# Performance work log

Hardware: AMD Instinct MI355X
Metric: run time of the kernel (lower is better)

The kernel has to match this reference:

```python
import jax, jax.numpy as jnp
import numpy as np

NEG_SLOPE = 0.2

def gat_conv(x, src, dst, W, a_src, a_dst, b, heads, out_ch, num_nodes):
    # Linear projection per head: [N, H, C]
    h = (x @ W).reshape(num_nodes, heads, out_ch)
    # Per-node attention logits: [N, H]
    s_src = jnp.sum(h * a_src[None, :, :], axis=-1)
    s_dst = jnp.sum(h * a_dst[None, :, :], axis=-1)
    # Per-edge attention score, LeakyReLU(0.2): [E, H]
    e = jax.nn.leaky_relu(s_src[src] + s_dst[dst], negative_slope=NEG_SLOPE)
    # Segment softmax over incoming edges of each destination node
    e_max = jax.ops.segment_max(e, dst, num_segments=num_nodes)
    e_exp = jnp.exp(e - e_max[dst])
    denom = jax.ops.segment_sum(e_exp, dst, num_segments=num_nodes)
    alpha = e_exp / (denom[dst] + 1e-16)  # [E, H]
    # Weighted message aggregation: [N, H, C]
    msg = h[src] * alpha[:, :, None]
    out = jax.ops.segment_sum(msg, dst, num_segments=num_nodes)
    # Concat heads + bias
    return out.reshape(num_nodes, heads * out_ch) + b


def setup_inputs() -> dict:
    key = jax.random.key(0)
    ks = jax.random.split(key, 9)
    N, E = 50000, 1000000
    x = jax.random.normal(ks[0], (N, 300), dtype=jnp.float32)
    edge_index = jax.random.randint(ks[1], (2, E), 0, N, dtype=jnp.int64)
    W1 = jax.random.normal(ks[2], (300, 64), dtype=jnp.float32) * 0.05
    a_src1 = jax.random.normal(ks[3], (8, 8), dtype=jnp.float32) * 0.1
    a_dst1 = jax.random.normal(ks[4], (8, 8), dtype=jnp.float32) * 0.1
    b1 = jnp.zeros((64,), dtype=jnp.float32)
    W2 = jax.random.normal(ks[5], (64, 64), dtype=jnp.float32) * 0.1
    a_src2 = jax.random.normal(ks[6], (1, 64), dtype=jnp.float32) * 0.1
    a_dst2 = jax.random.normal(ks[7], (1, 64), dtype=jnp.float32) * 0.1
    b2 = jnp.zeros((64,), dtype=jnp.float32)
    return {"x": x, "edge_index": edge_index, "W1": W1, "a_src1": a_src1,
            "a_dst1": a_dst1, "b1": b1, "W2": W2, "a_src2": a_src2,
            "a_dst2": a_dst2, "b2": b2}


def reference(x, edge_index, W1, a_src1, a_dst1, b1, W2, a_src2, a_dst2, b2):
    N = x.shape[0]
    src, dst = edge_index[0], edge_index[1]
    # eval mode: dropouts are identity
    h = gat_conv(x, src, dst, W1, a_src1, a_dst1, b1, heads=8, out_ch=8, num_nodes=N)
    h = jax.nn.elu(h)
    out = gat_conv(h, src, dst, W2, a_src2, a_dst2, b2, heads=1, out_ch=64, num_nodes=N)
    return out
```

## Files before the change

kernel.cpp:

```cpp
#include <hip/hip_runtime.h>
#include <math.h>

#define NN 50000
#define NE 1000000
#define EC 31
#define ECP 32
#define CSH 15
#define WR 8
#define RNG 6250
#define RPAD 6272
#define NCNT (EC * WR)
#define NGB 782

typedef __bf16 bf16x8 __attribute__((ext_vector_type(8)));
typedef float f32x4 __attribute__((ext_vector_type(4)));

__device__ inline unsigned short f2bf(float f) {
    unsigned u = __float_as_uint(f);
    u += 0x7FFFu + ((u >> 16) & 1u);
    return (unsigned short)(u >> 16);
}
__device__ inline float bf2f(unsigned short s) {
    return __uint_as_float(((unsigned)s) << 16);
}
__device__ inline float bflo(unsigned r) { return __uint_as_float(r << 16); }
__device__ inline float bfhi(unsigned r) { return __uint_as_float(r & 0xffff0000u); }

__global__ __launch_bounds__(256) void prep_init(const float* __restrict__ W1,
        const float* __restrict__ W2, unsigned short* __restrict__ Bt1,
        unsigned short* __restrict__ Bt2)
{
    int t = blockIdx.x * 256 + threadIdx.x;
    if (t < 64 * 320) {
        int c = t / 320, k = t % 320;
        Bt1[t] = (k < 300) ? f2bf(W1[k * 64 + c]) : (unsigned short)0;
    } else {
        int i = t - 64 * 320;
        int c = i >> 6, k = i & 63;
        Bt2[i] = f2bf(W2[k * 64 + c]);
    }
}

__global__ __launch_bounds__(1024) void k_count(
        const int* __restrict__ ei, int* __restrict__ cnt,
        unsigned char* __restrict__ pos)
{
    __shared__ __align__(16) int sm[RNG];
    const int tid = threadIdx.x;
    const int bid = blockIdx.x;
    const int c = bid >> 3, w = bid & 7;
    const int lo = w * RNG;
    for (int j = tid; j < RNG; j += 1024) sm[j] = 0;
    __syncthreads();
    const int base = c << CSH;
    #pragma unroll
    for (int it = 0; it < (1 << CSH) / 4096; ++it) {
        int e = base + (it * 1024 + tid) * 4;
        if (e < NE) {
            int4 d = *(const int4*)(ei + NE + e);
            unsigned t0 = (unsigned)(d.x - lo), t1 = (unsigned)(d.y - lo);
            unsigned t2 = (unsigned)(d.z - lo), t3 = (unsigned)(d.w - lo);
            if (t0 < RNG) pos[e]     = (unsigned char)atomicAdd(&sm[t0], 1);
            if (t1 < RNG) pos[e + 1] = (unsigned char)atomicAdd(&sm[t1], 1);
            if (t2 < RNG) pos[e + 2] = (unsigned char)atomicAdd(&sm[t2], 1);
            if (t3 < RNG) pos[e + 3] = (unsigned char)atomicAdd(&sm[t3], 1);
        }
    }
    __syncthreads();
    int* dstp = cnt + (size_t)bid * RPAD;
    for (int j = tid; j < RNG; j += 1024) dstp[j] = sm[j];
}

__global__ __launch_bounds__(256) void k_gemm(
        const float* __restrict__ A, const unsigned short* __restrict__ Bt,
        unsigned short* __restrict__ hb,
        const float* __restrict__ asrc, const float* __restrict__ adst,
        float* __restrict__ ss, float* __restrict__ sd)
{
    __shared__ unsigned short lds[5120];
    const int tid = threadIdx.x;
    const int row0 = blockIdx.x * 64;
    const int lane = tid & 63, w = tid >> 6;
    const int quad = lane >> 4, mm = lane & 15;
    const int sr = tid >> 2, q8 = (tid & 3) * 8;
    const int gsr = row0 + sr;
    const int K = 300, KT = 10, Kpad = 320, M = NN;

    f32x4 acc[4];
    #pragma unroll
    for (int i = 0; i < 4; ++i) acc[i] = (f32x4){0.f, 0.f, 0.f, 0.f};

    for (int kt = 0; kt < KT; ++kt) {
        const int k0 = kt * 32;
        int4 apack = {0, 0, 0, 0};
        if (gsr < M) {
            const float* ap = A + (size_t)gsr * K + k0 + q8;
            unsigned short* up = (unsigned short*)&apack;
            if (k0 + q8 + 7 < K) {
                float4 v0 = *(const float4*)ap;
                float4 v1 = *(const float4*)(ap + 4);
                up[0]=f2bf(v0.x); up[1]=f2bf(v0.y); up[2]=f2bf(v0.z); up[3]=f2bf(v0.w);
                up[4]=f2bf(v1.x); up[5]=f2bf(v1.y); up[6]=f2bf(v1.z); up[7]=f2bf(v1.w);
            } else {
                #pragma unroll
                for (int j = 0; j < 8; ++j)
                    up[j] = (k0 + q8 + j < K) ? f2bf(ap[j]) : (unsigned short)0;
            }
        }
        *(int4*)(lds + sr * 40 + q8) = apack;
        *(int4*)(lds + 2560 + sr * 40 + q8) =
            *(const int4*)(Bt + (size_t)sr * Kpad + k0 + q8);
        __syncthreads();
        bf16x8 af = *(const bf16x8*)(lds + (w * 16 + mm) * 40 + quad * 8);
        #pragma unroll
        for (int nt = 0; nt < 4; ++nt) {
            bf16x8 bfv = *(const bf16x8*)(lds + 2560 + (nt * 16 + mm) * 40 + quad * 8);
            acc[nt] = __builtin_amdgcn_mfma_f32_16x16x32_bf16(af, bfv, acc[nt], 0, 0, 0);
        }
        __syncthreads();
    }
    #pragma unroll
    for (int nt = 0; nt < 4; ++nt)
        #pragma unroll
        for (int reg = 0; reg < 4; ++reg)
            lds[w * 1152 + (quad * 4 + reg) * 72 + nt * 16 + mm] = f2bf(acc[nt][reg]);
    __syncthreads();
    const int cg = (tid & 3) * 16;
    const unsigned short* crow = lds + (sr >> 4) * 1152 + (sr & 15) * 72;
    if (gsr < M) {
        *(int4*)(hb + (size_t)gsr * 64 + cg)     = *(const int4*)(crow + cg);
        *(int4*)(hb + (size_t)gsr * 64 + cg + 8) = *(const int4*)(crow + cg + 8);
    }
    #pragma unroll
    for (int hh = 0; hh < 2; ++hh) {
        int hd = (tid & 3) + hh * 4;
        float pss = 0.f, psd = 0.f;
        #pragma unroll
        for (int c = 0; c < 8; ++c) {
            float hv = bf2f(crow[hd * 8 + c]);
            pss += hv * asrc[hd * 8 + c];
            psd += hv * adst[hd * 8 + c];
        }
        if (gsr < M) { ss[gsr * 8 + hd] = pss; sd[gsr * 8 + hd] = psd; }
    }
}

__global__ __launch_bounds__(256) void gemm_l2(const unsigned short* __restrict__ A,
        const unsigned short* __restrict__ Bt, unsigned short* __restrict__ hb,
        const float* __restrict__ asrc, const float* __restrict__ adst,
        float* __restrict__ ss, float* __restrict__ sd)
{
    __shared__ unsigned short lds[5120];
    const int tid  = threadIdx.x;
    const int row0 = blockIdx.x * 64;
    const int lane = tid & 63, w = tid >> 6;
    const int quad = lane >> 4, mm = lane & 15;
    const int sr = tid >> 2, q8 = (tid & 3) * 8;
    const int gsr = row0 + sr;
    const int K = 64, KT = 2, Kpad = 64, M = NN;

    f32x4 acc[4];
    #pragma unroll
    for (int i = 0; i < 4; ++i) acc[i] = (f32x4){0.f, 0.f, 0.f, 0.f};

    for (int kt = 0; kt < KT; ++kt) {
        const int k0 = kt * 32;
        int4 apack = {0, 0, 0, 0};
        if (gsr < M) apack = *(const int4*)(A + (size_t)gsr * K + k0 + q8);
        *(int4*)(lds + sr * 40 + q8) = apack;
        *(int4*)(lds + 2560 + sr * 40 + q8) =
            *(const int4*)(Bt + (size_t)sr * Kpad + k0 + q8);
        __syncthreads();
        bf16x8 af = *(const bf16x8*)(lds + (w * 16 + mm) * 40 + quad * 8);
        #pragma unroll
        for (int nt = 0; nt < 4; ++nt) {
            bf16x8 bfv = *(const bf16x8*)(lds + 2560 + (nt * 16 + mm) * 40 + quad * 8);
            acc[nt] = __builtin_amdgcn_mfma_f32_16x16x32_bf16(af, bfv, acc[nt], 0, 0, 0);
        }
        __syncthreads();
    }
    #pragma unroll
    for (int nt = 0; nt < 4; ++nt)
        #pragma unroll
        for (int reg = 0; reg < 4; ++reg)
            lds[w * 1152 + (quad * 4 + reg) * 72 + nt * 16 + mm] = f2bf(acc[nt][reg]);
    __syncthreads();
    const int cg = (tid & 3) * 16;
    const unsigned short* crow = lds + (sr >> 4) * 1152 + (sr & 15) * 72;
    if (gsr < M) {
        *(int4*)(hb + (size_t)gsr * 64 + cg)     = *(const int4*)(crow + cg);
        *(int4*)(hb + (size_t)gsr * 64 + cg + 8) = *(const int4*)(crow + cg + 8);
    }
    int p = tid & 3;
    float pss = 0.f, psd = 0.f;
    #pragma unroll
    for (int c = 0; c < 16; ++c) {
        float hv = bf2f(crow[p * 16 + c]);
        pss += hv * asrc[p * 16 + c];
        psd += hv * adst[p * 16 + c];
    }
    pss += __shfl_xor(pss, 1); psd += __shfl_xor(psd, 1);
    pss += __shfl_xor(pss, 2); psd += __shfl_xor(psd, 2);
    if (p == 0 && gsr < M) { ss[gsr] = pss; sd[gsr] = psd; }
}

__global__ __launch_bounds__(1024) void scan1(const int* __restrict__ cnt,
        int* __restrict__ excl, int* __restrict__ sums,
        unsigned char* __restrict__ rpre)
{
    __shared__ int buf[1024];
    int tid = threadIdx.x;
    int i = blockIdx.x * 1024 + tid;
    int v = 0;
    if (i < NN) {
        int w = i / RNG;
        int j = i - w * RNG;
        int run = 0;
        unsigned pk[ECP / 4];
        #pragma unroll
        for (int q = 0; q < ECP / 4; ++q) pk[q] = 0;
        #pragma unroll
        for (int c = 0; c < EC; ++c) {
            pk[c >> 2] |= ((unsigned)run & 0xffu) << ((c & 3) * 8);
            run += cnt[(size_t)(c * 8 + w) * RPAD + j];
        }
        v = run;
        *(uint4*)(rpre + (size_t)i * ECP)      = make_uint4(pk[0], pk[1], pk[2], pk[3]);
        *(uint4*)(rpre + (size_t)i * ECP + 16) = make_uint4(pk[4], pk[5], pk[6], pk[7]);
    }
    buf[tid] = v;
    __syncthreads();
    #pragma unroll
    for (int off = 1; off < 1024; off <<= 1) {
        int t = (tid >= off) ? buf[tid - off] : 0;
        __syncthreads();
        buf[tid] += t;
        __syncthreads();
    }
    if (i < NN) excl[i] = buf[tid] - v;
    if (tid == 1023) sums[blockIdx.x] = buf[1023];
}

__global__ __launch_bounds__(1024) void scan23(const int* __restrict__ excl,
        const int* __restrict__ sums, int* __restrict__ rowptr)
{
    int off = 0;
    for (int j = 0; j < (int)blockIdx.x; ++j) off += sums[j];
    int i = blockIdx.x * 1024 + threadIdx.x;
    if (i < NN) rowptr[i] = excl[i] + off;
    if (i == 0) rowptr[NN] = NE;
}

__global__ __launch_bounds__(256) void scatter_k(const int* __restrict__ ei,
        const int* __restrict__ rowptr, const unsigned char* __restrict__ pos,
        const unsigned char* __restrict__ rpre, unsigned short* __restrict__ col)
{
    int e = (blockIdx.x * 256 + threadIdx.x) * 4;
    if (e >= NE) return;
    int c = e >> CSH;
    int4 s = *(const int4*)(ei + e);
    int4 d = *(const int4*)(ei + NE + e);
    uchar4 p = *(const uchar4*)(pos + e);
    int r0 = rowptr[d.x] + (int)rpre[(d.x << 5) + c] + p.x;
    int r1 = rowptr[d.y] + (int)rpre[(d.y << 5) + c] + p.y;
    int r2 = rowptr[d.z] + (int)rpre[(d.z << 5) + c] + p.z;
    int r3 = rowptr[d.w] + (int)rpre[(d.w << 5) + c] + p.w;
    col[r0] = (unsigned short)s.x;
    col[r1] = (unsigned short)s.y;
    col[r2] = (unsigned short)s.z;
    col[r3] = (unsigned short)s.w;
}

#define LEAKY(s) ((s) > 0.f ? (s) : 0.2f * (s))

__global__ __launch_bounds__(256) void agg_l1(const int* __restrict__ rowptr,
        const unsigned short* __restrict__ col, const unsigned short* __restrict__ hb,
        const float* __restrict__ ss, const float* __restrict__ sd,
        const float* __restrict__ b, unsigned short* __restrict__ out)
{
    int n = (blockIdx.x * 256 + threadIdx.x) >> 6;
    int lane = threadIdx.x & 63;
    if (n >= NN) return;
    const int es = lane >> 4;
    const int cg = (lane & 15) << 2;
    const int hd = cg >> 3;
    float sdst = sd[n * 8 + hd];
    int r0 = rowptr[n], r1 = rowptr[n + 1];
    f32x4 acc = {0.f, 0.f, 0.f, 0.f};
    float dsum = 0.f;
    for (int i = r0; i < r1; i += 16) {
        int av[4]; bool vv[4];
        #pragma unroll
        for (int u = 0; u < 4; ++u) {
            int e = i + u * 4 + es;
            vv[u] = e < r1;
            av[u] = (int)col[vv[u] ? e : r0];
        }
        uint2 rr[4]; float sv[4];
        #pragma unroll
        for (int u = 0; u < 4; ++u) {
            rr[u] = *(const uint2*)(hb + av[u] * 64 + cg);
            sv[u] = ss[av[u] * 8 + hd];
        }
        #pragma unroll
        for (int u = 0; u < 4; ++u) {
            float wv = vv[u] ? __expf(LEAKY(sv[u] + sdst)) : 0.f;
            acc[0] += wv * bflo(rr[u].x);
            acc[1] += wv * bfhi(rr[u].x);
            acc[2] += wv * bflo(rr[u].y);
            acc[3] += wv * bfhi(rr[u].y);
            dsum += wv;
        }
    }
    #pragma unroll
    for (int m = 16; m <= 32; m <<= 1) {
        acc[0] += __shfl_xor(acc[0], m); acc[1] += __shfl_xor(acc[1], m);
        acc[2] += __shfl_xor(acc[2], m); acc[3] += __shfl_xor(acc[3], m);
        dsum += __shfl_xor(dsum, m);
    }
    if (es == 0) {
        float inv = 1.f / (dsum + 1e-16f);
        float v0 = acc[0] * inv + b[cg + 0]; v0 = v0 > 0.f ? v0 : __expf(v0) - 1.f;
        float v1 = acc[1] * inv + b[cg + 1]; v1 = v1 > 0.f ? v1 : __expf(v1) - 1.f;
        float v2 = acc[2] * inv + b[cg + 2]; v2 = v2 > 0.f ? v2 : __expf(v2) - 1.f;
        float v3 = acc[3] * inv + b[cg + 3]; v3 = v3 > 0.f ? v3 : __expf(v3) - 1.f;
        unsigned o01 = (unsigned)f2bf(v0) | ((unsigned)f2bf(v1) << 16);
        unsigned o23 = (unsigned)f2bf(v2) | ((unsigned)f2bf(v3) << 16);
        *(uint2*)(out + n * 64 + cg) = make_uint2(o01, o23);
    }
}

__global__ __launch_bounds__(256) void agg_l2(const int* __restrict__ rowptr,
        const unsigned short* __restrict__ col, const unsigned short* __restrict__ hb,
        const float* __restrict__ ss, const float* __restrict__ sd,
        const float* __restrict__ b, float* __restrict__ out)
{
    int n = (blockIdx.x * 256 + threadIdx.x) >> 6;
    int lane = threadIdx.x & 63;
    if (n >= NN) return;
    const int es = lane >> 4;
    const int cg = (lane & 15) << 2;
    float sdst = sd[n];
    int r0 = rowptr[n], r1 = rowptr[n + 1];
    f32x4 acc = {0.f, 0.f, 0.f, 0.f};
    float dsum = 0.f;
    for (int i = r0; i < r1; i += 16) {
        int av[4]; bool vv[4];
        #pragma unroll
        for (int u = 0; u < 4; ++u) {
            int e = i + u * 4 + es;
            vv[u] = e < r1;
            av[u] = (int)col[vv[u] ? e : r0];
        }
        uint2 rr[4]; float sv[4];
        #pragma unroll
        for (int u = 0; u < 4; ++u) {
            rr[u] = *(const uint2*)(hb + av[u] * 64 + cg);
            sv[u] = ss[av[u]];
        }
        #pragma unroll
        for (int u = 0; u < 4; ++u) {
            float wv = vv[u] ? __expf(LEAKY(sv[u] + sdst)) : 0.f;
            acc[0] += wv * bflo(rr[u].x);
            acc[1] += wv * bfhi(rr[u].x);
            acc[2] += wv * bflo(rr[u].y);
            acc[3] += wv * bfhi(rr[u].y);
            dsum += wv;
        }
    }
    #pragma unroll
    for (int m = 16; m <= 32; m <<= 1) {
        acc[0] += __shfl_xor(acc[0], m); acc[1] += __shfl_xor(acc[1], m);
        acc[2] += __shfl_xor(acc[2], m); acc[3] += __shfl_xor(acc[3], m);
        dsum += __shfl_xor(dsum, m);
    }
    if (es == 0) {
        float inv = 1.f / (dsum + 1e-16f);
        float4 o;
        o.x = acc[0] * inv + b[cg + 0];
        o.y = acc[1] * inv + b[cg + 1];
        o.z = acc[2] * inv + b[cg + 2];
        o.w = acc[3] * inv + b[cg + 3];
        *(float4*)(out + n * 64 + cg) = o;
    }
}

extern "C" void kernel_launch(void* const* d_in, const int* in_sizes, int n_in,
                              void* d_out, int out_size, void* d_ws, size_t ws_size,
                              hipStream_t stream)
{
    const float* x      = (const float*)d_in[0];
    const int*   ei     = (const int*)d_in[1];
    const float* W1     = (const float*)d_in[2];
    const float* a_src1 = (const float*)d_in[3];
    const float* a_dst1 = (const float*)d_in[4];
    const float* b1     = (const float*)d_in[5];
    const float* W2     = (const float*)d_in[6];
    const float* a_src2 = (const float*)d_in[7];
    const float* a_dst2 = (const float*)d_in[8];
    const float* b2     = (const float*)d_in[9];
    float* out = (float*)d_out;

    char* wp = (char*)d_ws;
    unsigned short* hb  = (unsigned short*)wp;  wp += (size_t)NN * 64 * 2;
    unsigned short* P1b = (unsigned short*)wp;  wp += (size_t)NN * 64 * 2;
    unsigned short* Bt1 = (unsigned short*)wp;  wp += (size_t)64 * 320 * 2;
    unsigned short* Bt2 = (unsigned short*)wp;  wp += (size_t)64 * 64 * 2;
    float* ss1 = (float*)wp;  wp += (size_t)NN * 8 * 4;
    float* sd1 = (float*)wp;  wp += (size_t)NN * 8 * 4;
    int* cnt    = (int*)wp;  wp += (size_t)NCNT * RPAD * 4;
    unsigned char* rpre = (unsigned char*)wp;  wp += (size_t)NN * ECP;
    int* excl   = (int*)wp;  wp += (size_t)NN * 4;
    int* sums   = (int*)wp;  wp += 64 * 4;
    int* rowptr = (int*)wp;  wp += (size_t)(NN + 4) * 4;
    unsigned short* col = (unsigned short*)wp;  wp += (size_t)(NE + 8) * 2;
    unsigned char*  pos = (unsigned char*)wp;   wp += (size_t)NE;
    float* ss2 = ss1;
    float* sd2 = ss1 + NN;

    const int NB = (NN + 1023) / 1024;

    prep_init<<<96, 256, 0, stream>>>(W1, W2, Bt1, Bt2);
    k_count<<<NCNT, 1024, 0, stream>>>(ei, cnt, pos);
    k_gemm<<<NGB, 256, 0, stream>>>(x, Bt1, hb, a_src1, a_dst1, ss1, sd1);
    scan1<<<NB, 1024, 0, stream>>>(cnt, excl, sums, rpre);
    scan23<<<NB, 1024, 0, stream>>>(excl, sums, rowptr);
    scatter_k<<<(NE / 4 + 255) / 256, 256, 0, stream>>>(ei, rowptr, pos, rpre, col);

    agg_l1<<<(NN * 64 + 255) / 256, 256, 0, stream>>>(rowptr, col, hb, ss1, sd1, b1, P1b);
    gemm_l2<<<(NN + 63) / 64, 256, 0, stream>>>(P1b, Bt2, hb, a_src2, a_dst2, ss2, sd2);
    agg_l2<<<(NN * 64 + 255) / 256, 256, 0, stream>>>(rowptr, col, hb, ss2, sd2, b2, out);
}
```

Baseline: 224.8 us.

## Fuse prep into count, scan into GEMM, widen K tiles and aggregation unroll

Merges the weight-transpose prep kernel into the edge-count kernel as extra blocks, and the first scan pass into the layer-1 GEMM launch as extra 256-thread blocks. scan23 is adjusted to the finer block sums. The GEMMs now process 64-wide K tiles, halving barrier rounds, and layer 2 drops its loop entirely. Both aggregation kernels issue 8 gathers per iteration instead of 4 for more memory-level parallelism. The cost is two fewer launches against more LDS and registers per block.

Result: no change. 223.4 us (-0.6%).

```diff
diff --git a/kernel.cpp b/kernel.cpp
--- a/kernel.cpp
+++ b/kernel.cpp
@@ -10,7 +10,9 @@
 #define RNG 6250
 #define RPAD 6272
 #define NCNT (EC * WR)
+#define NPB 24
 #define NGB 782
+#define NSB 196
 
 typedef __bf16 bf16x8 __attribute__((ext_vector_type(8)));
 typedef float f32x4 __attribute__((ext_vector_type(4)));
@@ -26,28 +28,28 @@
 __device__ inline float bflo(unsigned r) { return __uint_as_float(r << 16); }
 __device__ inline float bfhi(unsigned r) { return __uint_as_float(r & 0xffff0000u); }
 
-__global__ __launch_bounds__(256) void prep_init(const float* __restrict__ W1,
-        const float* __restrict__ W2, unsigned short* __restrict__ Bt1,
-        unsigned short* __restrict__ Bt2)
-{
-    int t = blockIdx.x * 256 + threadIdx.x;
-    if (t < 64 * 320) {
-        int c = t / 320, k = t % 320;
-        Bt1[t] = (k < 300) ? f2bf(W1[k * 64 + c]) : (unsigned short)0;
-    } else {
-        int i = t - 64 * 320;
-        int c = i >> 6, k = i & 63;
-        Bt2[i] = f2bf(W2[k * 64 + c]);
-    }
-}
-
-__global__ __launch_bounds__(1024) void k_count(
+__global__ __launch_bounds__(1024) void k_count_prep(
         const int* __restrict__ ei, int* __restrict__ cnt,
-        unsigned char* __restrict__ pos)
+        unsigned char* __restrict__ pos,
+        const float* __restrict__ W1, const float* __restrict__ W2,
+        unsigned short* __restrict__ Bt1, unsigned short* __restrict__ Bt2)
 {
     __shared__ __align__(16) int sm[RNG];
     const int tid = threadIdx.x;
     const int bid = blockIdx.x;
+
+    if (bid >= NCNT) {
+        int t = (bid - NCNT) * 1024 + tid;
+        if (t < 64 * 320) {
+            int c = t / 320, k = t % 320;
+            Bt1[t] = (k < 300) ? f2bf(W1[k * 64 + c]) : (unsigned short)0;
+        } else {
+            int i = t - 64 * 320;
+            int c = i >> 6, k = i & 63;
+            Bt2[i] = f2bf(W2[k * 64 + c]);
+        }
+        return;
+    }
     const int c = bid >> 3, w = bid & 7;
     const int lo = w * RNG;
     for (int j = tid; j < RNG; j += 1024) sm[j] = 0;
@@ -71,51 +73,104 @@
     for (int j = tid; j < RNG; j += 1024) dstp[j] = sm[j];
 }
 
-__global__ __launch_bounds__(256) void k_gemm(
+__global__ __launch_bounds__(256) void k_gemm_scan(
         const float* __restrict__ A, const unsigned short* __restrict__ Bt,
         unsigned short* __restrict__ hb,
         const float* __restrict__ asrc, const float* __restrict__ adst,
-        float* __restrict__ ss, float* __restrict__ sd)
-{
-    __shared__ unsigned short lds[5120];
+        float* __restrict__ ss, float* __restrict__ sd,
+        const int* __restrict__ cnt, int* __restrict__ excl,
+        int* __restrict__ sums, unsigned char* __restrict__ rpre)
+{
+    __shared__ __align__(16) unsigned short lds[9216];
     const int tid = threadIdx.x;
-    const int row0 = blockIdx.x * 64;
+    const int bid = blockIdx.x;
+
+    if (bid >= NGB) {
+        const int sb = bid - NGB;
+        int i = sb * 256 + tid;
+        int v = 0;
+        if (i < NN) {
+            int w8 = i / RNG;
+            int j = i - w8 * RNG;
+            int run = 0;
+            unsigned pk[ECP / 4];
+            #pragma unroll
+            for (int q = 0; q < ECP / 4; ++q) pk[q] = 0;
+            #pragma unroll
+            for (int cc = 0; cc < EC; ++cc) {
+                pk[cc >> 2] |= ((unsigned)run & 0xffu) << ((cc & 3) * 8);
+                run += cnt[(size_t)(cc * 8 + w8) * RPAD + j];
+            }
+            v = run;
+            *(uint4*)(rpre + (size_t)i * ECP)      = make_uint4(pk[0], pk[1], pk[2], pk[3]);
+            *(uint4*)(rpre + (size_t)i * ECP + 16) = make_uint4(pk[4], pk[5], pk[6], pk[7]);
+        }
+        int* buf = (int*)lds;
+        buf[tid] = v;
+        __syncthreads();
+        #pragma unroll
+        for (int off = 1; off < 256; off <<= 1) {
+            int t = (tid >= off) ? buf[tid - off] : 0;
+            __syncthreads();
+            buf[tid] += t;
+            __syncthreads();
+        }
+        if (i < NN) excl[i] = buf[tid] - v;
+        if (tid == 255) sums[sb] = buf[255];
+        return;
+    }
+
+    const int row0 = bid * 64;
     const int lane = tid & 63, w = tid >> 6;
     const int quad = lane >> 4, mm = lane & 15;
-    const int sr = tid >> 2, q8 = (tid & 3) * 8;
+    const int sr = tid >> 2, q16 = (tid & 3) * 16;
     const int gsr = row0 + sr;
-    const int K = 300, KT = 10, Kpad = 320, M = NN;
+    const int K = 300, M = NN;
 
     f32x4 acc[4];
     #pragma unroll
     for (int i = 0; i < 4; ++i) acc[i] = (f32x4){0.f, 0.f, 0.f, 0.f};
 
-    for (int kt = 0; kt < KT; ++kt) {
-        const int k0 = kt * 32;
-        int4 apack = {0, 0, 0, 0};
+    for (int kt = 0; kt < 5; ++kt) {
+        const int k0 = kt * 64;
+        int4 a0 = {0, 0, 0, 0}, a1 = {0, 0, 0, 0};
         if (gsr < M) {
-            const float* ap = A + (size_t)gsr * K + k0 + q8;
-            unsigned short* up = (unsigned short*)&apack;
-            if (k0 + q8 + 7 < K) {
+            const float* ap = A + (size_t)gsr * K + k0 + q16;
+            unsigned short* u0 = (unsigned short*)&a0;
+            unsigned short* u1 = (unsigned short*)&a1;
+            if (k0 + q16 + 15 < K) {
                 float4 v0 = *(const float4*)ap;
                 float4 v1 = *(const float4*)(ap + 4);
-                up[0]=f2bf(v0.x); up[1]=f2bf(v0.y); up[2]=f2bf(v0.z); up[3]=f2bf(v0.w);
-                up[4]=f2bf(v1.x); up[5]=f2bf(v1.y); up[6]=f2bf(v1.z); up[7]=f2bf(v1.w);
+                float4 v2 = *(const float4*)(ap + 8);
+                float4 v3 = *(const float4*)(ap + 12);
+                u0[0]=f2bf(v0.x); u0[1]=f2bf(v0.y); u0[2]=f2bf(v0.z); u0[3]=f2bf(v0.w);
+                u0[4]=f2bf(v1.x); u0[5]=f2bf(v1.y); u0[6]=f2bf(v1.z); u0[7]=f2bf(v1.w);
+                u1[0]=f2bf(v2.x); u1[1]=f2bf(v2.y); u1[2]=f2bf(v2.z); u1[3]=f2bf(v2.w);
+                u1[4]=f2bf(v3.x); u1[5]=f2bf(v3.y); u1[6]=f2bf(v3.z); u1[7]=f2bf(v3.w);
             } else {
                 #pragma unroll
                 for (int j = 0; j < 8; ++j)
-                    up[j] = (k0 + q8 + j < K) ? f2bf(ap[j]) : (unsigned short)0;
+                    u0[j] = (k0 + q16 + j < K) ? f2bf(ap[j]) : (unsigned short)0;
+                #pragma unroll
+                for (int j = 0; j < 8; ++j)
+                    u1[j] = (k0 + q16 + 8 + j < K) ? f2bf(ap[8 + j]) : (unsigned short)0;
             }
         }
-        *(int4*)(lds + sr * 40 + q8) = apack;
-        *(int4*)(lds + 2560 + sr * 40 + q8) =
-            *(const int4*)(Bt + (size_t)sr * Kpad + k0 + q8);
+        *(int4*)(lds + sr * 72 + q16)     = a0;
+        *(int4*)(lds + sr * 72 + q16 + 8) = a1;
+        *(int4*)(lds + 4608 + sr * 72 + q16) =
+            *(const int4*)(Bt + (size_t)sr * 320 + k0 + q16);
+        *(int4*)(lds + 4608 + sr * 72 + q16 + 8) =
+            *(const int4*)(Bt + (size_t)sr * 320 + k0 + q16 + 8);
         __syncthreads();
-        bf16x8 af = *(const bf16x8*)(lds + (w * 16 + mm) * 40 + quad * 8);
+        bf16x8 af0 = *(const bf16x8*)(lds + (w * 16 + mm) * 72 + quad * 8);
+        bf16x8 af1 = *(const bf16x8*)(lds + (w * 16 + mm) * 72 + 32 + quad * 8);
         #pragma unroll
         for (int nt = 0; nt < 4; ++nt) {
-            bf16x8 bfv = *(const bf16x8*)(lds + 2560 + (nt * 16 + mm) * 40 + quad * 8);
-            acc[nt] = __builtin_amdgcn_mfma_f32_16x16x32_bf16(af, bfv, acc[nt], 0, 0, 0);
+            bf16x8 b0 = *(const bf16x8*)(lds + 4608 + (nt * 16 + mm) * 72 + quad * 8);
+            bf16x8 b1 = *(const bf16x8*)(lds + 4608 + (nt * 16 + mm) * 72 + 32 + quad * 8);
+            acc[nt] = __builtin_amdgcn_mfma_f32_16x16x32_bf16(af0, b0, acc[nt], 0, 0, 0);
+            acc[nt] = __builtin_amdgcn_mfma_f32_16x16x32_bf16(af1, b1, acc[nt], 0, 0, 0);
         }
         __syncthreads();
     }
@@ -150,35 +205,38 @@
         const float* __restrict__ asrc, const float* __restrict__ adst,
         float* __restrict__ ss, float* __restrict__ sd)
 {
-    __shared__ unsigned short lds[5120];
+    __shared__ __align__(16) unsigned short lds[9216];
     const int tid  = threadIdx.x;
     const int row0 = blockIdx.x * 64;
     const int lane = tid & 63, w = tid >> 6;
     const int quad = lane >> 4, mm = lane & 15;
-    const int sr = tid >> 2, q8 = (tid & 3) * 8;
+    const int sr = tid >> 2, q16 = (tid & 3) * 16;
     const int gsr = row0 + sr;
-    const int K = 64, KT = 2, Kpad = 64, M = NN;
 
     f32x4 acc[4];
     #pragma unroll
     for (int i = 0; i < 4; ++i) acc[i] = (f32x4){0.f, 0.f, 0.f, 0.f};
 
-    for (int kt = 0; kt < KT; ++kt) {
-        const int k0 = kt * 32;
-        int4 apack = {0, 0, 0, 0};
-        if (gsr < M) apack = *(const int4*)(A + (size_t)gsr * K + k0 + q8);
-        *(int4*)(lds + sr * 40 + q8) = apack;
-        *(int4*)(lds + 2560 + sr * 40 + q8) =
-            *(const int4*)(Bt + (size_t)sr * Kpad + k0 + q8);
-        __syncthreads();
-        bf16x8 af = *(const bf16x8*)(lds + (w * 16 + mm) * 40 + quad * 8);
-        #pragma unroll
-        for (int nt = 0; nt < 4; ++nt) {
-            bf16x8 bfv = *(const bf16x8*)(lds + 2560 + (nt * 16 + mm) * 40 + quad * 8);
-            acc[nt] = __builtin_amdgcn_mfma_f32_16x16x32_bf16(af, bfv, acc[nt], 0, 0, 0);
-        }
-        __syncthreads();
-    }
+    int4 a0 = {0, 0, 0, 0}, a1 = {0, 0, 0, 0};
+    if (gsr < NN) {
+        a0 = *(const int4*)(A + (size_t)gsr * 64 + q16);
+        a1 = *(const int4*)(A + (size_t)gsr * 64 + q16 + 8);
+    }
+    *(int4*)(lds + sr * 72 + q16)     = a0;
+    *(int4*)(lds + sr * 72 + q16 + 8) = a1;
+    *(int4*)(lds + 4608 + sr * 72 + q16)     = *(const int4*)(Bt + sr * 64 + q16);
+    *(int4*)(lds + 4608 + sr * 72 + q16 + 8) = *(const int4*)(Bt + sr * 64 + q16 + 8);
+    __syncthreads();
+    bf16x8 af0 = *(const bf16x8*)(lds + (w * 16 + mm) * 72 + quad * 8);
+    bf16x8 af1 = *(const bf16x8*)(lds + (w * 16 + mm) * 72 + 32 + quad * 8);
+    #pragma unroll
+    for (int nt = 0; nt < 4; ++nt) {
+        bf16x8 b0 = *(const bf16x8*)(lds + 4608 + (nt * 16 + mm) * 72 + quad * 8);
+        bf16x8 b1 = *(const bf16x8*)(lds + 4608 + (nt * 16 + mm) * 72 + 32 + quad * 8);
+        acc[nt] = __builtin_amdgcn_mfma_f32_16x16x32_bf16(af0, b0, acc[nt], 0, 0, 0);
+        acc[nt] = __builtin_amdgcn_mfma_f32_16x16x32_bf16(af1, b1, acc[nt], 0, 0, 0);
+    }
+    __syncthreads();
     #pragma unroll
     for (int nt = 0; nt < 4; ++nt)
         #pragma unroll
@@ -187,7 +245,7 @@
     __syncthreads();
     const int cg = (tid & 3) * 16;
     const unsigned short* crow = lds + (sr >> 4) * 1152 + (sr & 15) * 72;
-    if (gsr < M) {
+    if (gsr < NN) {
         *(int4*)(hb + (size_t)gsr * 64 + cg)     = *(const int4*)(crow + cg);
         *(int4*)(hb + (size_t)gsr * 64 + cg + 8) = *(const int4*)(crow + cg + 8);
     }
@@ -201,52 +259,18 @@
     }
     pss += __shfl_xor(pss, 1); psd += __shfl_xor(psd, 1);
     pss += __shfl_xor(pss, 2); psd += __shfl_xor(psd, 2);
-    if (p == 0 && gsr < M) { ss[gsr] = pss; sd[gsr] = psd; }
-}
-
-__global__ __launch_bounds__(1024) void scan1(const int* __restrict__ cnt,
-        int* __restrict__ excl, int* __restrict__ sums,
-        unsigned char* __restrict__ rpre)
-{
-    __shared__ int buf[1024];
-    int tid = threadIdx.x;
-    int i = blockIdx.x * 1024 + tid;
-    int v = 0;
-    if (i < NN) {
-        int w = i / RNG;
-        int j = i - w * RNG;
-        int run = 0;
-        unsigned pk[ECP / 4];
-        #pragma unroll
-        for (int q = 0; q < ECP / 4; ++q) pk[q] = 0;
-        #pragma unroll
-        for (int c = 0; c < EC; ++c) {
-            pk[c >> 2] |= ((unsigned)run & 0xffu) << ((c & 3) * 8);
-            run += cnt[(size_t)(c * 8 + w) * RPAD + j];
-        }
-        v = run;
-        *(uint4*)(rpre + (size_t)i * ECP)      = make_uint4(pk[0], pk[1], pk[2], pk[3]);
-        *(uint4*)(rpre + (size_t)i * ECP + 16) = make_uint4(pk[4], pk[5], pk[6], pk[7]);
-    }
-    buf[tid] = v;
-    __syncthreads();
-    #pragma unroll
-    for (int off = 1; off < 1024; off <<= 1) {
-        int t = (tid >= off) ? buf[tid - off] : 0;
-        __syncthreads();
-        buf[tid] += t;
-        __syncthreads();
-    }
-    if (i < NN) excl[i] = buf[tid] - v;
-    if (tid == 1023) sums[blockIdx.x] = buf[1023];
+    if (p == 0 && gsr < NN) { ss[gsr] = pss; sd[gsr] = psd; }
 }
 
 __global__ __launch_bounds__(1024) void scan23(const int* __restrict__ excl,
         const int* __restrict__ sums, int* __restrict__ rowptr)
 {
+    int blk = (int)blockIdx.x * 4;
     int off = 0;
-    for (int j = 0; j < (int)blockIdx.x; ++j) off += sums[j];
-    int i = blockIdx.x * 1024 + threadIdx.x;
+    for (int j = 0; j < blk; ++j) off += sums[j];
+    int sub = (threadIdx.x >> 8);
+    for (int j = 0; j < sub; ++j) off += sums[blk + j];
+    int i = (int)blockIdx.x * 1024 + threadIdx.x;
     if (i < NN) rowptr[i] = excl[i] + off;
     if (i == 0) rowptr[NN] = NE;
 }
@@ -288,22 +312,22 @@
     int r0 = rowptr[n], r1 = rowptr[n + 1];
     f32x4 acc = {0.f, 0.f, 0.f, 0.f};
     float dsum = 0.f;
-    for (int i = r0; i < r1; i += 16) {
-        int av[4]; bool vv[4];
-        #pragma unroll
-        for (int u = 0; u < 4; ++u) {
+    for (int i = r0; i < r1; i += 32) {
+        int av[8]; bool vv[8];
+        #pragma unroll
+        for (int u = 0; u < 8; ++u) {
             int e = i + u * 4 + es;
             vv[u] = e < r1;
             av[u] = (int)col[vv[u] ? e : r0];
         }
-        uint2 rr[4]; float sv[4];
-        #pragma unroll
-        for (int u = 0; u < 4; ++u) {
+        uint2 rr[8]; float sv[8];
+        #pragma unroll
+        for (int u = 0; u < 8; ++u) {
             rr[u] = *(const uint2*)(hb + av[u] * 64 + cg);
             sv[u] = ss[av[u] * 8 + hd];
         }
         #pragma unroll
-        for (int u = 0; u < 4; ++u) {
+        for (int u = 0; u < 8; ++u) {
             float wv = vv[u] ? __expf(LEAKY(sv[u] + sdst)) : 0.f;
             acc[0] += wv * bflo(rr[u].x);
             acc[1] += wv * bfhi(rr[u].x);
@@ -344,22 +368,22 @@
     int r0 = rowptr[n], r1 = rowptr[n + 1];
     f32x4 acc = {0.f, 0.f, 0.f, 0.f};
     float dsum = 0.f;
-    for (int i = r0; i < r1; i += 16) {
-        int av[4]; bool vv[4];
-        #pragma unroll
-        for (int u = 0; u < 4; ++u) {
+    for (int i = r0; i < r1; i += 32) {
+        int av[8]; bool vv[8];
+        #pragma unroll
+        for (int u = 0; u < 8; ++u) {
             int e = i + u * 4 + es;
             vv[u] = e < r1;
             av[u] = (int)col[vv[u] ? e : r0];
         }
-        uint2 rr[4]; float sv[4];
-        #pragma unroll
-        for (int u = 0; u < 4; ++u) {
+        uint2 rr[8]; float sv[8];
+        #pragma unroll
+        for (int u = 0; u < 8; ++u) {
             rr[u] = *(const uint2*)(hb + av[u] * 64 + cg);
             sv[u] = ss[av[u]];
         }
         #pragma unroll
-        for (int u = 0; u < 4; ++u) {
+        for (int u = 0; u < 8; ++u) {
             float wv = vv[u] ? __expf(LEAKY(sv[u] + sdst)) : 0.f;
             acc[0] += wv * bflo(rr[u].x);
             acc[1] += wv * bfhi(rr[u].x);
@@ -411,7 +435,7 @@
     int* cnt    = (int*)wp;  wp += (size_t)NCNT * RPAD * 4;
     unsigned char* rpre = (unsigned char*)wp;  wp += (size_t)NN * ECP;
     int* excl   = (int*)wp;  wp += (size_t)NN * 4;
-    int* sums   = (int*)wp;  wp += 64 * 4;
+    int* sums   = (int*)wp;  wp += 256 * 4;
     int* rowptr = (int*)wp;  wp += (size_t)(NN + 4) * 4;
     unsigned short* col = (unsigned short*)wp;  wp += (size_t)(NE + 8) * 2;
     unsigned char*  pos = (unsigned char*)wp;   wp += (size_t)NE;
@@ -420,10 +444,9 @@
 
     const int NB = (NN + 1023) / 1024;
 
-    prep_init<<<96, 256, 0, stream>>>(W1, W2, Bt1, Bt2);
-    k_count<<<NCNT, 1024, 0, stream>>>(ei, cnt, pos);
-    k_gemm<<<NGB, 256, 0, stream>>>(x, Bt1, hb, a_src1, a_dst1, ss1, sd1);
-    scan1<<<NB, 1024, 0, stream>>>(cnt, excl, sums, rpre);
+    k_count_prep<<<NCNT + NPB, 1024, 0, stream>>>(ei, cnt, pos, W1, W2, Bt1, Bt2);
+    k_gemm_scan<<<NGB + NSB, 256, 0, stream>>>(
+        x, Bt1, hb, a_src1, a_dst1, ss1, sd1, cnt, excl, sums, rpre);
     scan23<<<NB, 1024, 0, stream>>>(excl, sums, rowptr);
     scatter_k<<<(NE / 4 + 255) / 256, 256, 0, stream>>>(ei, rowptr, pos, rpre, col);
 
```
